# Optimization experiments

Hardware: AMD Instinct MI355X
Metric: run time of the kernel (lower is better)

## Reference

```python
import jax, jax.numpy as jnp
import numpy as np

B, N = 8, 65536
REG_WEIGHT = 1.0


def box2corners(box):
    # box: (B,N,5) [x,y,w,h,alpha] -> corners (B,N,4,2), CCW order
    x, y, w, h, alpha = (box[..., i] for i in range(5))
    x4 = jnp.asarray([0.5, -0.5, -0.5, 0.5], box.dtype) * w[..., None]
    y4 = jnp.asarray([0.5, 0.5, -0.5, -0.5], box.dtype) * h[..., None]
    c = jnp.cos(alpha)[..., None]
    s = jnp.sin(alpha)[..., None]
    cx = x4 * c - y4 * s + x[..., None]
    cy = x4 * s + y4 * c + y[..., None]
    return jnp.stack([cx, cy], axis=-1)


def box_intersection(c1, c2):
    # all 4x4 edge-pair intersections -> pts (B,N,16,2), mask (B,N,16)
    p1, q1 = c1, jnp.roll(c1, -1, axis=2)
    p2, q2 = c2, jnp.roll(c2, -1, axis=2)
    x1, y1 = p1[..., :, None, 0], p1[..., :, None, 1]
    x2, y2 = q1[..., :, None, 0], q1[..., :, None, 1]
    x3, y3 = p2[..., None, :, 0], p2[..., None, :, 1]
    x4, y4 = q2[..., None, :, 0], q2[..., None, :, 1]
    den = (x4 - x3) * (y1 - y2) - (x1 - x2) * (y4 - y3)
    num_t = (y4 - y3) * (x1 - x3) - (x4 - x3) * (y1 - y3)
    num_u = (y1 - y2) * (x1 - x3) - (x1 - x2) * (y1 - y3)
    safe = jnp.where(den == 0, 1.0, den)
    t = jnp.where(den == 0, -1.0, num_t / safe)
    u = jnp.where(den == 0, -1.0, -num_u / safe)
    mask = (t > 0) & (t < 1) & (u > 0) & (u < 1)
    pts = jnp.stack([x1 + t * (x2 - x1), y1 + t * (y2 - y1)], axis=-1)
    pts = pts * mask[..., None]
    Bb, Nn = c1.shape[0], c1.shape[1]
    return pts.reshape(Bb, Nn, 16, 2), mask.reshape(Bb, Nn, 16)


def box1_in_box2(c1, c2):
    # corners of box1 (B,N,4,2) inside box2 via projection on its edges
    a, b, d = c2[..., 0:1, :], c2[..., 1:2, :], c2[..., 3:4, :]
    ab, ad, ap = b - a, d - a, c1 - a
    pab = jnp.sum(ap * ab, -1) / jnp.sum(ab * ab, -1)
    pad_ = jnp.sum(ap * ad, -1) / jnp.sum(ad * ad, -1)
    eps = 1e-6
    return (pab > -eps) & (pab < 1 + eps) & (pad_ > -eps) & (pad_ < 1 + eps)


def oriented_box_intersection_2d(c1, c2):
    pts, m_i = box_intersection(c1, c2)
    m1 = box1_in_box2(c1, c2)
    m2 = box1_in_box2(c2, c1)
    verts = jnp.concatenate([c1, c2, pts], axis=2)   # (B,N,24,2)
    mask = jnp.concatenate([m1, m2, m_i], axis=2)    # (B,N,24)
    mf = mask[..., None].astype(verts.dtype)
    nv = jnp.maximum(jnp.sum(mf, axis=2, keepdims=True), 1.0)
    mean = jnp.sum(verts * mf, axis=2, keepdims=True) / nv  # (B,N,1,2)
    dxy = verts - mean
    ang = jnp.where(mask, jnp.arctan2(dxy[..., 1], dxy[..., 0]), 1e9)
    order = jnp.argsort(ang, axis=-1)
    sv = jnp.take_along_axis(verts, order[..., None], axis=2)
    sm = jnp.take_along_axis(mask, order, axis=-1)
    # pad invalid slots with the first (smallest-angle) valid vertex -> zero shoelace contribution
    poly = jnp.where(sm[..., None], sv, sv[..., 0:1, :])
    x, y = poly[..., 0], poly[..., 1]
    area = 0.5 * jnp.abs(jnp.sum(x * jnp.roll(y, -1, axis=-1) - jnp.roll(x, -1, axis=-1) * y, axis=-1))
    return area, poly


def diff_iou_rotated_3d(box3d1, box3d2, mode='iou'):
    idx = jnp.asarray([0, 1, 3, 4, 6])
    c1 = box2corners(box3d1[..., idx])
    c2 = box2corners(box3d2[..., idx])
    inter_2d, _ = oriented_box_intersection_2d(c1, c2)
    zmax1 = box3d1[..., 2] + 0.5 * box3d1[..., 5]
    zmin1 = box3d1[..., 2] - 0.5 * box3d1[..., 5]
    zmax2 = box3d2[..., 2] + 0.5 * box3d2[..., 5]
    zmin2 = box3d2[..., 2] - 0.5 * box3d2[..., 5]
    z_overlap = jnp.clip(jnp.minimum(zmax1, zmax2) - jnp.maximum(zmin1, zmin2), 0.0)
    inter_3d = inter_2d * z_overlap
    vol1 = box3d1[..., 3] * box3d1[..., 4] * box3d1[..., 5]
    vol2 = box3d2[..., 3] * box3d2[..., 4] * box3d2[..., 5]
    union = vol1 + vol2 - inter_3d
    iou = inter_3d / union
    if mode == 'iou':
        return iou
    inter_diag = jnp.sum((box3d1[..., 0:3] - box3d2[..., 0:3]) ** 2, axis=-1)
    outer_h = jnp.clip(jnp.maximum(zmax1, zmax2) - jnp.minimum(zmin1, zmin2), 0.0)
    out_max = jnp.maximum(c1[:, :, 2], c2[:, :, 2])
    out_min = jnp.minimum(c1[:, :, 0], c2[:, :, 0])
    outer = jnp.clip(out_max - out_min, 0.0)
    outer_diag = outer[..., 0] ** 2 + outer[..., 1] ** 2 + outer_h ** 2
    return jnp.clip(iou - inter_diag / outer_diag, -1.0, 1.0)


def setup_inputs() -> dict:
    key = jax.random.key(0)
    ks = jax.random.split(key, 5)
    ctr = jax.random.uniform(ks[0], (B, N, 3), minval=-50.0, maxval=50.0)
    dims = jax.random.uniform(ks[1], (B, N, 3), minval=1.0, maxval=5.0)
    ang = jax.random.uniform(ks[2], (B, N, 1), minval=-np.pi, maxval=np.pi)
    pred_boxes = jnp.concatenate([ctr, dims, ang], axis=-1)  # (B,N,7)
    noise = jax.random.normal(ks[3], (B, N, 7)) * jnp.asarray([0.5, 0.5, 0.3, 0.3, 0.3, 0.3, 0.2])
    gt7 = pred_boxes + noise
    gt_dims = jnp.maximum(gt7[..., 3:6], 0.1)
    gt_boxes = jnp.concatenate([gt7[..., :3], gt_dims, jnp.sin(gt7[..., 6:7]), jnp.cos(gt7[..., 6:7])], axis=-1)  # (B,N,8)
    pred_iou = jax.random.uniform(ks[4], (B, N)) * 2.0 - 1.0
    mask = jnp.ones((B, N), dtype=bool)
    return {'pred_iou': pred_iou, 'pred_boxes': pred_boxes, 'gt_boxes': gt_boxes, 'mask': mask}


def reference(pred_iou, pred_boxes, gt_boxes, mask):
    mf = mask.astype(pred_iou.dtype).reshape(-1)
    cnt = jnp.maximum(jnp.sum(mf), 1e-4)
    Bb, Nn = pred_iou.shape
    pb = pred_boxes.reshape(1, Bb * Nn, 7)
    gb = gt_boxes.reshape(1, Bb * Nn, 8)
    ang = jnp.arctan2(gb[..., 6:7], gb[..., 7:8])
    gb7 = jnp.concatenate([gb[..., :6], ang], axis=-1)
    target = diff_iou_rotated_3d(pb, gb7, 'iou').reshape(-1) * 2.0 - 1.0
    iou_loss = jnp.sum(jnp.abs(pred_iou.reshape(-1) - target) * mf) / cnt
    diou = diff_iou_rotated_3d(pb, gb7, 'diou').reshape(-1)
    reg_loss = jnp.sum((1.0 - diou) * mf) / cnt
    return iou_loss + reg_loss * REG_WEIGHT
```

## Files before the change

kernel.cpp:

```cpp
#include <hip/hip_runtime.h>


#define RCPF(x) __builtin_amdgcn_rcpf(x)

__device__ __forceinline__ unsigned sortKey(float f) {
    unsigned u = __float_as_uint(f);
    return (u & 0x80000000u) ? ~u : (u | 0x80000000u);
}

struct EIn {
    float b[7];
    float g[8];
    float pred;
    float mf;
};

__device__ __forceinline__ void load_elem(EIn& e,
    const float* __restrict__ pred_iou, const float* __restrict__ pred_boxes,
    const float* __restrict__ gt_boxes, const int* __restrict__ mask,
    int gid, bool active)
{
    const float* pb = pred_boxes + (size_t)gid * 7;
    #pragma unroll
    for (int k = 0; k < 7; ++k) e.b[k] = pb[k];
    const float4 g0 = reinterpret_cast<const float4*>(gt_boxes)[(size_t)gid * 2 + 0];
    const float4 g1 = reinterpret_cast<const float4*>(gt_boxes)[(size_t)gid * 2 + 1];
    e.g[0] = g0.x; e.g[1] = g0.y; e.g[2] = g0.z; e.g[3] = g0.w;
    e.g[4] = g1.x; e.g[5] = g1.y; e.g[6] = g1.z; e.g[7] = g1.w;
    e.pred = pred_iou[gid];
    e.mf = (active && mask[gid] != 0) ? 1.0f : 0.0f;
}

__device__ __forceinline__ float elem_body(const EIn& e,
    float* __restrict__ X, float* __restrict__ Y)
{
    const float b1x = e.b[0], b1y = e.b[1], b1z = e.b[2];
    const float b1w = e.b[3], b1h = e.b[4], b1l = e.b[5], a1 = e.b[6];
    const float b2x = e.g[0], b2y = e.g[1], b2z = e.g[2];
    const float b2w = e.g[3], b2h = e.g[4], b2l = e.g[5];
    const float gsn = e.g[6], gcs = e.g[7];

    float sn1, cs1;
    __sincosf(a1, &sn1, &cs1);
    const float rn = __builtin_amdgcn_rsqf(gsn * gsn + gcs * gcs);
    const float sn2 = gsn * rn, cs2 = gcs * rn;

    const float xs[4] = {0.5f, -0.5f, -0.5f, 0.5f};
    const float ys[4] = {0.5f, 0.5f, -0.5f, -0.5f};
    float c1x[4], c1y[4], c2x[4], c2y[4];
    #pragma unroll
    for (int k = 0; k < 4; ++k) {
        float xx = xs[k] * b1w, yy = ys[k] * b1h;
        c1x[k] = xx * cs1 - yy * sn1 + b1x;
        c1y[k] = xx * sn1 + yy * cs1 + b1y;
        float x2 = xs[k] * b2w, y2 = ys[k] * b2h;
        c2x[k] = x2 * cs2 - y2 * sn2 + b2x;
        c2y[k] = x2 * sn2 + y2 * cs2 + b2y;
    }

    unsigned r = 0u;
    const float eps = 1e-6f;

    {
        float ax = c2x[0], ay = c2y[0];
        float abx = c2x[1] - ax, aby = c2y[1] - ay;
        float adx = c2x[3] - ax, ady = c2y[3] - ay;
        float ab2 = abx * abx + aby * aby;
        float ad2 = adx * adx + ady * ady;
        float lo_ab = -eps * ab2, hi_ab = (1.0f + eps) * ab2;
        float lo_ad = -eps * ad2, hi_ad = (1.0f + eps) * ad2;
        #pragma unroll
        for (int k = 0; k < 4; ++k) {
            float apx = c1x[k] - ax, apy = c1y[k] - ay;
            float dab = apx * abx + apy * aby;
            float dad = apx * adx + apy * ady;
            bool ok = (dab > lo_ab) && (dab < hi_ab) && (dad > lo_ad) && (dad < hi_ad);
            unsigned rm = r < 8u ? r : 8u;
            X[rm * 256] = c1x[k];
            Y[rm * 256] = c1y[k];
            r += ok ? 1u : 0u;
        }
    }
    {
        float ax = c1x[0], ay = c1y[0];
        float abx = c1x[1] - ax, aby = c1y[1] - ay;
        float adx = c1x[3] - ax, ady = c1y[3] - ay;
        float ab2 = abx * abx + aby * aby;
        float ad2 = adx * adx + ady * ady;
        float lo_ab = -eps * ab2, hi_ab = (1.0f + eps) * ab2;
        float lo_ad = -eps * ad2, hi_ad = (1.0f + eps) * ad2;
        #pragma unroll
        for (int k = 0; k < 4; ++k) {
            float apx = c2x[k] - ax, apy = c2y[k] - ay;
            float dab = apx * abx + apy * aby;
            float dad = apx * adx + apy * ady;
            bool ok = (dab > lo_ab) && (dab < hi_ab) && (dad > lo_ad) && (dad < hi_ad);
            unsigned rm = r < 8u ? r : 8u;
            X[rm * 256] = c2x[k];
            Y[rm * 256] = c2y[k];
            r += ok ? 1u : 0u;
        }
    }
    float e1dx[4], e1dy[4], e2dx[4], e2dy[4];
    #pragma unroll
    for (int l = 0; l < 4; ++l) {
        e1dx[l] = c1x[l] - c1x[(l + 1) & 3];
        e1dy[l] = c1y[l] - c1y[(l + 1) & 3];
        e2dx[l] = c2x[l] - c2x[(l + 1) & 3];
        e2dy[l] = c2y[l] - c2y[(l + 1) & 3];
    }
    #pragma unroll
    for (int l = 0; l < 4; ++l) {
        float x1 = c1x[l], y1 = c1y[l];
        #pragma unroll
        for (int m = 0; m < 4; ++m) {
            float rx = x1 - c2x[m], ry = y1 - c2y[m];
            float den  = e1dx[l] * e2dy[m] - e2dx[m] * e1dy[l];
            float numt = e2dx[m] * ry - e2dy[m] * rx;
            float numu = e1dx[l] * ry - e1dy[l] * rx;
            float aden = fabsf(den);
            bool ok = (numt * den > 0.0f) && (fabsf(numt) < aden) &&
                      (numu * den > 0.0f) && (fabsf(numu) < aden);
            float t = numt * RCPF(den);
            float Xc = x1 - t * e1dx[l];
            float Yc = y1 - t * e1dy[l];
            unsigned rm = r < 8u ? r : 8u;
            X[rm * 256] = Xc;
            Y[rm * 256] = Yc;
            r += ok ? 1u : 0u;
        }
    }

    float px[8], py[8];
    #pragma unroll
    for (int j = 0; j < 8; ++j) {
        px[j] = X[j * 256];
        py[j] = Y[j * 256];
    }
    int kcnt = (int)(r < 8u ? r : 8u);

    float sxm = 0.0f, sym = 0.0f;
    #pragma unroll
    for (int j = 0; j < 8; ++j) {
        bool a = (j < kcnt);
        sxm += a ? px[j] : 0.0f;
        sym += a ? py[j] : 0.0f;
    }
    float rnv = RCPF(fmaxf((float)kcnt, 1.0f));
    float mx = sxm * rnv, my = sym * rnv;

    unsigned key[8];
    #pragma unroll
    for (int j = 0; j < 8; ++j) {
        float dx = px[j] - mx, dy = py[j] - my;
        float ad = fabsf(dx) + fabsf(dy);
        float rr = dx * RCPF(fmaxf(ad, 1e-30f));
        float k = __builtin_copysignf(1.0f - rr, dy);
        float kf = (j < kcnt) ? k : 1e9f;
        key[j] = (sortKey(kf) & 0xFFFFFFF8u) | (unsigned)j;
    }

    #define CE(a, b) { unsigned lo = min(key[a], key[b]); \
                       unsigned hi = max(key[a], key[b]); \
                       key[a] = lo; key[b] = hi; }
    CE(0,1) CE(2,3) CE(4,5) CE(6,7)
    CE(0,2) CE(1,3) CE(4,6) CE(5,7)
    CE(1,2) CE(5,6)
    CE(0,4) CE(1,5) CE(2,6) CE(3,7)
    CE(2,4) CE(3,5)
    CE(1,2) CE(3,4) CE(5,6)
    #undef CE

    float sx[8], sy[8];
    #pragma unroll
    for (int j = 0; j < 8; ++j) {
        unsigned idx = key[j] & 7u;
        sx[j] = X[idx * 256];
        sy[j] = Y[idx * 256];
    }

    float x0 = sx[0], y0 = sy[0];
    float area2 = 0.0f;
    #pragma unroll
    for (int v = 0; v < 8; ++v) {
        bool act = (v < kcnt);
        bool wrap = (v + 1 == kcnt);
        float nx2 = (v == 7) ? x0 : (wrap ? x0 : sx[v + 1]);
        float ny2 = (v == 7) ? y0 : (wrap ? y0 : sy[v + 1]);
        float term = sx[v] * ny2 - nx2 * sy[v];
        area2 += act ? term : 0.0f;
    }
    float inter2d = 0.5f * fabsf(area2);

    float zmax1 = b1z + 0.5f * b1l, zmin1 = b1z - 0.5f * b1l;
    float zmax2 = b2z + 0.5f * b2l, zmin2 = b2z - 0.5f * b2l;
    float zov = fmaxf(fminf(zmax1, zmax2) - fmaxf(zmin1, zmin2), 0.0f);
    float inter3d = inter2d * zov;
    float vol1 = b1w * b1h * b1l;
    float vol2 = b2w * b2h * b2l;
    float uni = vol1 + vol2 - inter3d;
    float iou = inter3d * RCPF(uni);
    float target = iou * 2.0f - 1.0f;

    float ddx = b1x - b2x, ddy = b1y - b2y, ddz = b1z - b2z;
    float interdiag = ddx * ddx + ddy * ddy + ddz * ddz;
    float outerh = fmaxf(fmaxf(zmax1, zmax2) - fminf(zmin1, zmin2), 0.0f);
    float omx = fmaxf(fmaxf(c1x[2], c2x[2]) - fminf(c1x[0], c2x[0]), 0.0f);
    float omy = fmaxf(fmaxf(c1y[2], c2y[2]) - fminf(c1y[0], c2y[0]), 0.0f);
    float outerdiag = omx * omx + omy * omy + outerh * outerh;
    float diou = iou - interdiag * RCPF(outerdiag);
    diou = fminf(fmaxf(diou, -1.0f), 1.0f);

    return (fabsf(e.pred - target) + (1.0f - diou)) * e.mf;
}

__global__ __launch_bounds__(256, 4) void iou3d_loss_kernel(
    const float* __restrict__ pred_iou,
    const float* __restrict__ pred_boxes,
    const float* __restrict__ gt_boxes,
    const int*   __restrict__ mask,
    float* __restrict__ sums,
    int M)
{
    __shared__ float sX[2][9][256];
    __shared__ float sY[2][9][256];
    float* X0 = &sX[0][0][threadIdx.x];
    float* Y0 = &sY[0][0][threadIdx.x];
    float* X1 = &sX[1][0][threadIdx.x];
    float* Y1 = &sY[1][0][threadIdx.x];

    const int idx0 = blockIdx.x * blockDim.x + threadIdx.x;
    const int stride = gridDim.x * blockDim.x;
    const int idx1 = idx0 + stride;
    const int mlast = M - 1;
    const int i0 = idx0 < M ? idx0 : mlast;
    const int i1 = idx1 < M ? idx1 : mlast;

    EIn e0, e1;
    load_elem(e0, pred_iou, pred_boxes, gt_boxes, mask, i0, idx0 < M);
    load_elem(e1, pred_iou, pred_boxes, gt_boxes, mask, i1, idx1 < M);
    float contrib = elem_body(e0, X0, Y0) + elem_body(e1, X1, Y1);
    float mfv = e0.mf + e1.mf;

    #pragma unroll
    for (int off = 32; off > 0; off >>= 1) {
        contrib += __shfl_down(contrib, off, 64);
        mfv     += __shfl_down(mfv, off, 64);
    }
    __shared__ float sC[4], sM[4];
    const int lane = threadIdx.x & 63;
    const int wv = threadIdx.x >> 6;
    if (lane == 0) { sC[wv] = contrib; sM[wv] = mfv; }
    __syncthreads();
    if (threadIdx.x == 0) {
        float tc = sC[0] + sC[1] + sC[2] + sC[3];
        float tm = sM[0] + sM[1] + sM[2] + sM[3];
        atomicAdd(&sums[0], tc);
        atomicAdd(&sums[1], tm);
    }
}

__global__ void finalize_kernel(const float* __restrict__ sums, float* __restrict__ out) {
    if (threadIdx.x == 0 && blockIdx.x == 0)
        out[0] = sums[0] / fmaxf(sums[1], 1e-4f);
}

extern "C" void kernel_launch(void* const* d_in, const int* in_sizes, int n_in,
                              void* d_out, int out_size, void* d_ws, size_t ws_size,
                              hipStream_t stream) {
    const float* pred_iou   = (const float*)d_in[0];
    const float* pred_boxes = (const float*)d_in[1];
    const float* gt_boxes   = (const float*)d_in[2];
    const int*   mask       = (const int*)d_in[3];
    float* out  = (float*)d_out;
    float* sums = (float*)d_ws;
    const int M = in_sizes[0];

    hipMemsetAsync(sums, 0, 2 * sizeof(float), stream);
    const int block = 256;
    const int elems_per_thread = 2;
    int grid = (M + block * elems_per_thread - 1) / (block * elems_per_thread);
    if (grid < 1) grid = 1;
    hipLaunchKernelGGL(iou3d_loss_kernel, dim3(grid), dim3(block), 0, stream,
                       pred_iou, pred_boxes, gt_boxes, mask, sums, M);
    hipLaunchKernelGGL(finalize_kernel, dim3(1), dim3(64), 0, stream, sums, out);
}
```

Before: 113.5 us.

## Compute box intersection in box1's local frame to simplify edge tests

Moves the polygon-intersection geometry into box1's axis-aligned local frame, so box1's corners are ±half extents and box2 is rotated by the relative angle. Containment tests become abs-comparisons, and the sixteen edge-pair intersections reuse a few precomputed products and reciprocals instead of doing a general determinant and reciprocal each. The aim is to cut ALU work and register pressure in the per-element body. The shoelace area is unchanged by the rigid transform. The risk is small floating-point and epsilon-boundary differences in the inside and intersection predicates.

Measured after the change: 112.0 us. No clear change (-1.4%).

```diff
diff --git a/kernel.cpp b/kernel.cpp
--- a/kernel.cpp
+++ b/kernel.cpp
@@ -3,9 +3,20 @@
 
 #define RCPF(x) __builtin_amdgcn_rcpf(x)
 
-__device__ __forceinline__ unsigned sortKey(float f) {
+__device__ __forceinline__ unsigned sortKeyU(float f) {
     unsigned u = __float_as_uint(f);
     return (u & 0x80000000u) ? ~u : (u | 0x80000000u);
+}
+
+__device__ __forceinline__ void sort8(unsigned k[8]) {
+#define CE(a, b) { unsigned lo = min(k[a], k[b]); unsigned hi = max(k[a], k[b]); k[a] = lo; k[b] = hi; }
+    CE(0,1) CE(2,3) CE(4,5) CE(6,7)
+    CE(0,2) CE(1,3) CE(4,6) CE(5,7)
+    CE(1,2) CE(5,6)
+    CE(0,4) CE(1,5) CE(2,6) CE(3,7)
+    CE(2,4) CE(3,5)
+    CE(1,2) CE(3,4) CE(5,6)
+#undef CE
 }
 
 struct EIn {
@@ -34,102 +45,134 @@
 __device__ __forceinline__ float elem_body(const EIn& e,
     float* __restrict__ X, float* __restrict__ Y)
 {
-    const float b1x = e.b[0], b1y = e.b[1], b1z = e.b[2];
-    const float b1w = e.b[3], b1h = e.b[4], b1l = e.b[5], a1 = e.b[6];
-    const float b2x = e.g[0], b2y = e.g[1], b2z = e.g[2];
-    const float b2w = e.g[3], b2h = e.g[4], b2l = e.g[5];
+    const float bx = e.b[0], by = e.b[1], bz = e.b[2];
+    const float w1 = e.b[3], h1 = e.b[4], l1 = e.b[5], a1 = e.b[6];
+    const float gx = e.g[0], gy = e.g[1], gz = e.g[2];
+    const float w2 = e.g[3], h2 = e.g[4], l2 = e.g[5];
     const float gsn = e.g[6], gcs = e.g[7];
 
     float sn1, cs1;
     __sincosf(a1, &sn1, &cs1);
     const float rn = __builtin_amdgcn_rsqf(gsn * gsn + gcs * gcs);
     const float sn2 = gsn * rn, cs2 = gcs * rn;
-
-    const float xs[4] = {0.5f, -0.5f, -0.5f, 0.5f};
-    const float ys[4] = {0.5f, 0.5f, -0.5f, -0.5f};
-    float c1x[4], c1y[4], c2x[4], c2y[4];
-    #pragma unroll
-    for (int k = 0; k < 4; ++k) {
-        float xx = xs[k] * b1w, yy = ys[k] * b1h;
-        c1x[k] = xx * cs1 - yy * sn1 + b1x;
-        c1y[k] = xx * sn1 + yy * cs1 + b1y;
-        float x2 = xs[k] * b2w, y2 = ys[k] * b2h;
-        c2x[k] = x2 * cs2 - y2 * sn2 + b2x;
-        c2y[k] = x2 * sn2 + y2 * cs2 + b2y;
-    }
+    const float cs21 = cs2 * cs1 + sn2 * sn1;
+    const float sn21 = sn2 * cs1 - cs2 * sn1;
+
+    const float hw1 = 0.5f * w1, hh1 = 0.5f * h1;
+    const float hw2 = 0.5f * w2, hh2 = 0.5f * h2;
+    const float nhw1 = -hw1, nhh1 = -hh1;
+
+    const float cdx = gx - bx, cdy = gy - by;
+    const float d1x = cdx * cs1 + cdy * sn1;
+    const float d1y = cdy * cs1 - cdx * sn1;
+
+    const float ru = hw2 * cs21, rv = hh2 * sn21;
+    const float rp = hw2 * sn21, rq = hh2 * cs21;
+    float Bx[4], By[4];
+    Bx[0] = d1x + ru - rv;  By[0] = d1y + rp + rq;
+    Bx[1] = d1x - ru - rv;  By[1] = d1y - rp + rq;
+    Bx[2] = d1x - ru + rv;  By[2] = d1y - rp - rq;
+    Bx[3] = d1x + ru + rv;  By[3] = d1y + rp - rq;
+
+    const float e2x0 = w2 * cs21,    e2y0 = w2 * sn21;
+    const float e2x1 = -(h2 * sn21), e2y1 = h2 * cs21;
+    const float ae2x0 = fabsf(e2x0), ae2y0 = fabsf(e2y0);
+    const float ae2x1 = fabsf(e2x1), ae2y1 = fabsf(e2y1);
+    const float P0 = w1 * e2y0, P1 = w1 * e2y1;
+    const float Q0 = h1 * e2x0, Q1 = h1 * e2x1;
+    const float aP0 = fabsf(P0), aP1 = fabsf(P1);
+    const float aQ0 = fabsf(Q0), aQ1 = fabsf(Q1);
+    const float rP0 = RCPF(P0), rP1 = RCPF(P1);
+    const float rQ0 = RCPF(Q0), rQ1 = RCPF(Q1);
+
+    const float eps = 1e-6f;
+    const float tx1 = hw1 + eps * w1, ty1 = hh1 + eps * h1;
+    const float tx2 = hw2 + eps * w2, ty2 = hh2 + eps * h2;
 
     unsigned r = 0u;
-    const float eps = 1e-6f;
+#define EMIT(xv, yv, ok) { unsigned rm = r < 8u ? r : 8u; \
+                           X[rm * 256] = (xv); Y[rm * 256] = (yv); \
+                           r += (ok) ? 1u : 0u; }
 
     {
-        float ax = c2x[0], ay = c2y[0];
-        float abx = c2x[1] - ax, aby = c2y[1] - ay;
-        float adx = c2x[3] - ax, ady = c2y[3] - ay;
-        float ab2 = abx * abx + aby * aby;
-        float ad2 = adx * adx + ady * ady;
-        float lo_ab = -eps * ab2, hi_ab = (1.0f + eps) * ab2;
-        float lo_ad = -eps * ad2, hi_ad = (1.0f + eps) * ad2;
+        const float uxp = hw1 - d1x, uxm = nhw1 - d1x;
+        const float uyp = hh1 - d1y, uym = nhh1 - d1y;
         #pragma unroll
         for (int k = 0; k < 4; ++k) {
-            float apx = c1x[k] - ax, apy = c1y[k] - ay;
-            float dab = apx * abx + apy * aby;
-            float dad = apx * adx + apy * ady;
-            bool ok = (dab > lo_ab) && (dab < hi_ab) && (dad > lo_ad) && (dad < hi_ad);
-            unsigned rm = r < 8u ? r : 8u;
-            X[rm * 256] = c1x[k];
-            Y[rm * 256] = c1y[k];
-            r += ok ? 1u : 0u;
+            const float ux = (k == 0 || k == 3) ? uxp : uxm;
+            const float uy = (k < 2) ? uyp : uym;
+            const float ax2 = ux * cs21 + uy * sn21;
+            const float ay2 = uy * cs21 - ux * sn21;
+            const float Axv = (k == 0 || k == 3) ? hw1 : nhw1;
+            const float Ayv = (k < 2) ? hh1 : nhh1;
+            const bool ok = fabsf(ax2) < tx2 && fabsf(ay2) < ty2;
+            EMIT(Axv, Ayv, ok)
         }
     }
     {
-        float ax = c1x[0], ay = c1y[0];
-        float abx = c1x[1] - ax, aby = c1y[1] - ay;
-        float adx = c1x[3] - ax, ady = c1y[3] - ay;
-        float ab2 = abx * abx + aby * aby;
-        float ad2 = adx * adx + ady * ady;
-        float lo_ab = -eps * ab2, hi_ab = (1.0f + eps) * ab2;
-        float lo_ad = -eps * ad2, hi_ad = (1.0f + eps) * ad2;
         #pragma unroll
         for (int k = 0; k < 4; ++k) {
-            float apx = c2x[k] - ax, apy = c2y[k] - ay;
-            float dab = apx * abx + apy * aby;
-            float dad = apx * adx + apy * ady;
-            bool ok = (dab > lo_ab) && (dab < hi_ab) && (dad > lo_ad) && (dad < hi_ad);
-            unsigned rm = r < 8u ? r : 8u;
-            X[rm * 256] = c2x[k];
-            Y[rm * 256] = c2y[k];
-            r += ok ? 1u : 0u;
+            const bool ok = fabsf(Bx[k]) < tx1 && fabsf(By[k]) < ty1;
+            EMIT(Bx[k], By[k], ok)
         }
     }
-    float e1dx[4], e1dy[4], e2dx[4], e2dy[4];
-    #pragma unroll
-    for (int l = 0; l < 4; ++l) {
-        e1dx[l] = c1x[l] - c1x[(l + 1) & 3];
-        e1dy[l] = c1y[l] - c1y[(l + 1) & 3];
-        e2dx[l] = c2x[l] - c2x[(l + 1) & 3];
-        e2dy[l] = c2y[l] - c2y[(l + 1) & 3];
-    }
-    #pragma unroll
-    for (int l = 0; l < 4; ++l) {
-        float x1 = c1x[l], y1 = c1y[l];
-        #pragma unroll
-        for (int m = 0; m < 4; ++m) {
-            float rx = x1 - c2x[m], ry = y1 - c2y[m];
-            float den  = e1dx[l] * e2dy[m] - e2dx[m] * e1dy[l];
-            float numt = e2dx[m] * ry - e2dy[m] * rx;
-            float numu = e1dx[l] * ry - e1dy[l] * rx;
-            float aden = fabsf(den);
-            bool ok = (numt * den > 0.0f) && (fabsf(numt) < aden) &&
-                      (numu * den > 0.0f) && (fabsf(numu) < aden);
-            float t = numt * RCPF(den);
-            float Xc = x1 - t * e1dx[l];
-            float Yc = y1 - t * e1dy[l];
-            unsigned rm = r < 8u ? r : 8u;
-            X[rm * 256] = Xc;
-            Y[rm * 256] = Yc;
-            r += ok ? 1u : 0u;
-        }
-    }
+    #pragma unroll
+    for (int m = 0; m < 4; ++m) {
+        const bool bb = m & 1; const bool mp = m < 2;
+        const float e2xb = bb ? e2x1 : e2x0, e2yb = bb ? e2y1 : e2y0;
+        const float aeyb = bb ? ae2y1 : ae2y0;
+        const float Pb = bb ? P1 : P0, aPb = bb ? aP1 : aP0, rPb = bb ? rP1 : rP0;
+        const float rx = hw1 - Bx[m], ry = hh1 - By[m];
+        const float nt = e2xb * ry - e2yb * rx;
+        const float q1 = nt * Pb, q2 = ry * e2yb;
+        const float Xv = hw1 - (nt * rPb) * w1;
+        const bool ok = (q1 > 0.0f) && (fabsf(nt) < aPb) &&
+                        (mp ? q2 > 0.0f : q2 < 0.0f) && (fabsf(ry) < aeyb);
+        EMIT(Xv, hh1, ok)
+    }
+    #pragma unroll
+    for (int m = 0; m < 4; ++m) {
+        const bool bb = m & 1; const bool mp = m < 2;
+        const float e2xb = bb ? e2x1 : e2x0, e2yb = bb ? e2y1 : e2y0;
+        const float aexb = bb ? ae2x1 : ae2x0;
+        const float Qb = bb ? Q1 : Q0, aQb = bb ? aQ1 : aQ0, rQb = bb ? rQ1 : rQ0;
+        const float rx = nhw1 - Bx[m], ry = hh1 - By[m];
+        const float nt = e2xb * ry - e2yb * rx;
+        const float q1 = nt * Qb, q2 = rx * e2xb;
+        const float Yv = hh1 + (nt * rQb) * h1;
+        const bool ok = (q1 < 0.0f) && (fabsf(nt) < aQb) &&
+                        (mp ? q2 > 0.0f : q2 < 0.0f) && (fabsf(rx) < aexb);
+        EMIT(nhw1, Yv, ok)
+    }
+    #pragma unroll
+    for (int m = 0; m < 4; ++m) {
+        const bool bb = m & 1; const bool mp = m < 2;
+        const float e2xb = bb ? e2x1 : e2x0, e2yb = bb ? e2y1 : e2y0;
+        const float aeyb = bb ? ae2y1 : ae2y0;
+        const float Pb = bb ? P1 : P0, aPb = bb ? aP1 : aP0, rPb = bb ? rP1 : rP0;
+        const float rx = nhw1 - Bx[m], ry = nhh1 - By[m];
+        const float nt = e2xb * ry - e2yb * rx;
+        const float q1 = nt * Pb, q2 = ry * e2yb;
+        const float Xv = nhw1 - (nt * rPb) * w1;
+        const bool ok = (q1 < 0.0f) && (fabsf(nt) < aPb) &&
+                        (mp ? q2 > 0.0f : q2 < 0.0f) && (fabsf(ry) < aeyb);
+        EMIT(Xv, nhh1, ok)
+    }
+    #pragma unroll
+    for (int m = 0; m < 4; ++m) {
+        const bool bb = m & 1; const bool mp = m < 2;
+        const float e2xb = bb ? e2x1 : e2x0, e2yb = bb ? e2y1 : e2y0;
+        const float aexb = bb ? ae2x1 : ae2x0;
+        const float Qb = bb ? Q1 : Q0, aQb = bb ? aQ1 : aQ0, rQb = bb ? rQ1 : rQ0;
+        const float rx = hw1 - Bx[m], ry = nhh1 - By[m];
+        const float nt = e2xb * ry - e2yb * rx;
+        const float q1 = nt * Qb, q2 = rx * e2xb;
+        const float Yv = nhh1 + (nt * rQb) * h1;
+        const bool ok = (q1 > 0.0f) && (fabsf(nt) < aQb) &&
+                        (mp ? q2 > 0.0f : q2 < 0.0f) && (fabsf(rx) < aexb);
+        EMIT(hw1, Yv, ok)
+    }
+#undef EMIT
 
     float px[8], py[8];
     #pragma unroll
@@ -137,77 +180,66 @@
         px[j] = X[j * 256];
         py[j] = Y[j * 256];
     }
-    int kcnt = (int)(r < 8u ? r : 8u);
-
+    const int kcnt = (int)(r < 8u ? r : 8u);
     float sxm = 0.0f, sym = 0.0f;
     #pragma unroll
     for (int j = 0; j < 8; ++j) {
-        bool a = (j < kcnt);
+        const bool a = (j < kcnt);
         sxm += a ? px[j] : 0.0f;
         sym += a ? py[j] : 0.0f;
     }
-    float rnv = RCPF(fmaxf((float)kcnt, 1.0f));
-    float mx = sxm * rnv, my = sym * rnv;
+    const float rnv = RCPF(fmaxf((float)kcnt, 1.0f));
+    const float mx = sxm * rnv, my = sym * rnv;
 
     unsigned key[8];
     #pragma unroll
     for (int j = 0; j < 8; ++j) {
-        float dx = px[j] - mx, dy = py[j] - my;
-        float ad = fabsf(dx) + fabsf(dy);
-        float rr = dx * RCPF(fmaxf(ad, 1e-30f));
-        float k = __builtin_copysignf(1.0f - rr, dy);
-        float kf = (j < kcnt) ? k : 1e9f;
-        key[j] = (sortKey(kf) & 0xFFFFFFF8u) | (unsigned)j;
-    }
-
-    #define CE(a, b) { unsigned lo = min(key[a], key[b]); \
-                       unsigned hi = max(key[a], key[b]); \
-                       key[a] = lo; key[b] = hi; }
-    CE(0,1) CE(2,3) CE(4,5) CE(6,7)
-    CE(0,2) CE(1,3) CE(4,6) CE(5,7)
-    CE(1,2) CE(5,6)
-    CE(0,4) CE(1,5) CE(2,6) CE(3,7)
-    CE(2,4) CE(3,5)
-    CE(1,2) CE(3,4) CE(5,6)
-    #undef CE
+        const float dx = px[j] - mx, dy = py[j] - my;
+        const float ad = fabsf(dx) + fabsf(dy);
+        const float rr = dx * RCPF(fmaxf(ad, 1e-30f));
+        float kf = __builtin_copysignf(1.0f - rr, dy);
+        kf = (j < kcnt) ? kf : 1e9f;
+        key[j] = (sortKeyU(kf) & 0xFFFFFFF8u) | (unsigned)j;
+    }
+    sort8(key);
 
     float sx[8], sy[8];
     #pragma unroll
     for (int j = 0; j < 8; ++j) {
-        unsigned idx = key[j] & 7u;
+        const unsigned idx = key[j] & 7u;
         sx[j] = X[idx * 256];
         sy[j] = Y[idx * 256];
     }
-
-    float x0 = sx[0], y0 = sy[0];
+    const float x0 = sx[0], y0 = sy[0];
     float area2 = 0.0f;
     #pragma unroll
     for (int v = 0; v < 8; ++v) {
-        bool act = (v < kcnt);
-        bool wrap = (v + 1 == kcnt);
-        float nx2 = (v == 7) ? x0 : (wrap ? x0 : sx[v + 1]);
-        float ny2 = (v == 7) ? y0 : (wrap ? y0 : sy[v + 1]);
-        float term = sx[v] * ny2 - nx2 * sy[v];
+        const bool act = (v < kcnt);
+        const bool wrap = (v + 1 == kcnt);
+        const float nx2 = (v == 7) ? x0 : (wrap ? x0 : sx[v + 1]);
+        const float ny2 = (v == 7) ? y0 : (wrap ? y0 : sy[v + 1]);
+        const float term = sx[v] * ny2 - nx2 * sy[v];
         area2 += act ? term : 0.0f;
     }
-    float inter2d = 0.5f * fabsf(area2);
-
-    float zmax1 = b1z + 0.5f * b1l, zmin1 = b1z - 0.5f * b1l;
-    float zmax2 = b2z + 0.5f * b2l, zmin2 = b2z - 0.5f * b2l;
-    float zov = fmaxf(fminf(zmax1, zmax2) - fmaxf(zmin1, zmin2), 0.0f);
-    float inter3d = inter2d * zov;
-    float vol1 = b1w * b1h * b1l;
-    float vol2 = b2w * b2h * b2l;
-    float uni = vol1 + vol2 - inter3d;
-    float iou = inter3d * RCPF(uni);
-    float target = iou * 2.0f - 1.0f;
-
-    float ddx = b1x - b2x, ddy = b1y - b2y, ddz = b1z - b2z;
-    float interdiag = ddx * ddx + ddy * ddy + ddz * ddz;
-    float outerh = fmaxf(fmaxf(zmax1, zmax2) - fminf(zmin1, zmin2), 0.0f);
-    float omx = fmaxf(fmaxf(c1x[2], c2x[2]) - fminf(c1x[0], c2x[0]), 0.0f);
-    float omy = fmaxf(fmaxf(c1y[2], c2y[2]) - fminf(c1y[0], c2y[0]), 0.0f);
-    float outerdiag = omx * omx + omy * omy + outerh * outerh;
+    const float inter2d = 0.5f * fabsf(area2);
+
+    const float zmax1 = bz + 0.5f * l1, zmin1 = bz - 0.5f * l1;
+    const float zmax2 = gz + 0.5f * l2, zmin2 = gz - 0.5f * l2;
+    const float zov = fmaxf(fminf(zmax1, zmax2) - fmaxf(zmin1, zmin2), 0.0f);
+    const float inter3d = inter2d * zov;
+    const float vol1 = w1 * h1 * l1, vol2 = w2 * h2 * l2;
+    const float uni = vol1 + vol2 - inter3d;
+    const float iou = inter3d * RCPF(uni);
+    const float target = iou * 2.0f - 1.0f;
+
+    const float ddx = bx - gx, ddy = by - gy, ddz = bz - gz;
+    const float interdiag = ddx * ddx + ddy * ddy + ddz * ddz;
+    const float v1x = hw1 * cs1 - hh1 * sn1, v1y = hw1 * sn1 + hh1 * cs1;
+    const float w2x = hw2 * cs2 - hh2 * sn2, w2y = hw2 * sn2 + hh2 * cs2;
+    const float outerh = fmaxf(fmaxf(zmax1, zmax2) - fminf(zmin1, zmin2), 0.0f);
+    const float omx = fmaxf(fmaxf(bx - v1x, gx - w2x) - fminf(bx + v1x, gx + w2x), 0.0f);
+    const float omy = fmaxf(fmaxf(by - v1y, gy - w2y) - fminf(by + v1y, gy + w2y), 0.0f);
+    const float outerdiag = omx * omx + omy * omy + outerh * outerh;
     float diou = iou - interdiag * RCPF(outerdiag);
     diou = fminf(fmaxf(diou, -1.0f), 1.0f);
 
@@ -222,19 +254,20 @@
     float* __restrict__ sums,
     int M)
 {
-    __shared__ float sX[2][9][256];
-    __shared__ float sY[2][9][256];
-    float* X0 = &sX[0][0][threadIdx.x];
-    float* Y0 = &sY[0][0][threadIdx.x];
-    float* X1 = &sX[1][0][threadIdx.x];
-    float* Y1 = &sY[1][0][threadIdx.x];
-
-    const int idx0 = blockIdx.x * blockDim.x + threadIdx.x;
+    __shared__ float sXs[2][9][256];
+    __shared__ float sYs[2][9][256];
+    const int tid = threadIdx.x;
+    float* X0 = &sXs[0][0][tid];
+    float* Y0 = &sYs[0][0][tid];
+    float* X1 = &sXs[1][0][tid];
+    float* Y1 = &sYs[1][0][tid];
+
+    const int idx0 = blockIdx.x * blockDim.x + tid;
     const int stride = gridDim.x * blockDim.x;
     const int idx1 = idx0 + stride;
-    const int mlast = M - 1;
-    const int i0 = idx0 < M ? idx0 : mlast;
-    const int i1 = idx1 < M ? idx1 : mlast;
+    const int ml = M - 1;
+    const int i0 = idx0 < M ? idx0 : ml;
+    const int i1 = idx1 < M ? idx1 : ml;
 
     EIn e0, e1;
     load_elem(e0, pred_iou, pred_boxes, gt_boxes, mask, i0, idx0 < M);
@@ -248,11 +281,11 @@
         mfv     += __shfl_down(mfv, off, 64);
     }
     __shared__ float sC[4], sM[4];
-    const int lane = threadIdx.x & 63;
-    const int wv = threadIdx.x >> 6;
+    const int lane = tid & 63;
+    const int wv = tid >> 6;
     if (lane == 0) { sC[wv] = contrib; sM[wv] = mfv; }
     __syncthreads();
-    if (threadIdx.x == 0) {
+    if (tid == 0) {
         float tc = sC[0] + sC[1] + sC[2] + sC[3];
         float tm = sM[0] + sM[1] + sM[2] + sM[3];
         atomicAdd(&sums[0], tc);
```
